# Performance work log

Measured on AMD Instinct MI355X. Metric: run time of the kernel, lower is better.

## Reference

```python
import jax, jax.numpy as jnp
import numpy as np

N, NPG, BS = 32000, 1000, 32
E, H, L, R, K = 512000, 128, 3, 8, 64


def setup_inputs() -> dict:
    key = jax.random.key(0)
    ks = jax.random.split(key, 16)
    sc = 0.05
    x = jax.random.normal(ks[0], (N, H), jnp.float32)
    W_rel = jax.random.normal(ks[1], (L, R, H, H), jnp.float32) * sc
    W_self = jax.random.normal(ks[2], (L, H, H), jnp.float32) * sc
    rel_table = jax.random.normal(ks[3], (R, H), jnp.float32)
    Zn = jax.random.normal(ks[4], (K, H), jnp.float32) * sc
    proj_W = jax.random.normal(ks[5], (L * H, H), jnp.float32) * sc
    proj_b = jnp.zeros((H,), jnp.float32)
    fc_W = jax.random.normal(ks[6], (2 * L * H + 2 * H, 1), jnp.float32) * sc
    fc_b = jnp.zeros((1,), jnp.float32)
    rep_seq = jax.random.normal(ks[7], (BS, H), jnp.float32)
    src = jax.random.randint(ks[8], (E,), 0, N, jnp.int32)
    dst = jax.random.randint(ks[9], (E,), 0, N, jnp.int32)
    etype = jax.random.randint(ks[10], (E,), 0, R, jnp.int32)
    graph_id = (jnp.arange(N, dtype=jnp.int32) // NPG).astype(jnp.int32)
    head_ids = (jnp.arange(BS, dtype=jnp.int32) * NPG)           # node with id==1 per subgraph
    tail_ids = (jnp.arange(BS, dtype=jnp.int32) * NPG + 1)       # node with id==2 per subgraph
    rel_labels = jax.random.randint(ks[11], (BS,), 0, R, jnp.int32)
    return dict(x=x, W_rel=W_rel, W_self=W_self, rel_table=rel_table, Zn=Zn,
                proj_W=proj_W, proj_b=proj_b, fc_W=fc_W, fc_b=fc_b, rep_seq=rep_seq,
                src=src, dst=dst, etype=etype, graph_id=graph_id,
                head_ids=head_ids, tail_ids=tail_ids, rel_labels=rel_labels)


def reference(x, W_rel, W_self, rel_table, Zn, proj_W, proj_b, fc_W, fc_b, rep_seq,
              src, dst, etype, graph_id, head_ids, tail_ids, rel_labels):
    n, h_dim = x.shape
    bs = head_ids.shape[0]
    # RGCN message passing: aggregate src features per (dst, rel), then per-rel linear.
    seg = dst.astype(jnp.int32) * R + etype.astype(jnp.int32)  # [E]
    h = x
    reprs = []
    for l in range(L):
        agg = jax.ops.segment_sum(h[src], seg, num_segments=n * R)  # [N*R, H]
        agg = agg.reshape(n, R, h_dim)
        msg = jnp.einsum('nri,rio->no', agg, W_rel[l])
        h = jax.nn.relu(msg + h @ W_self[l])
        reprs.append(h)
    repr_ = jnp.stack(reprs, axis=1)  # [N, L, H]
    # mean_nodes pooling per subgraph
    counts = jax.ops.segment_sum(jnp.ones((n,), x.dtype), graph_id, num_segments=bs)
    g_mean = jax.ops.segment_sum(repr_, graph_id, num_segments=bs) / counts[:, None, None]
    g_out = jax.nn.leaky_relu(g_mean.reshape(bs, L * h_dim) @ proj_W + proj_b)  # [bs, H]
    # head/tail gathers
    head_flat = repr_[head_ids].reshape(bs, L * h_dim)
    tail_flat = repr_[tail_ids].reshape(bs, L * h_dim)
    rel_embs = rel_table[rel_labels]  # [bs, H]
    h_out = head_flat @ proj_W + proj_b
    t_out = tail_flat @ proj_W + proj_b
    # community view: cluster assignment (softmax) then summary (sigmoid)
    s1 = jax.nn.sigmoid(jax.nn.softmax(h_out @ Zn.T, axis=-1) @ Zn)
    s2 = jax.nn.sigmoid(jax.nn.softmax(t_out @ Zn.T, axis=-1) @ Zn)
    s = s1 * s2
    # view attention aggregation over [subgraph, sequence, community] views
    views = jnp.stack([g_out, rep_seq, s], axis=1)  # [bs, 3, H]
    att = jax.nn.softmax(jnp.sum(rel_embs[:, None, :] * views, axis=-1), axis=-1)  # [bs, 3]
    view_aggr = jnp.sum(att[:, :, None] * views, axis=1)  # [bs, H]
    # positive triplet scoring
    g_rep = jnp.concatenate([head_flat, tail_flat, rel_embs, view_aggr], axis=1)
    out_pos = g_rep @ fc_W + fc_b  # [bs, 1]
    return out_pos
```

## Files before the change

### kernel.cpp

```cpp
#include <hip/hip_runtime.h>

#define N_NODES 32000
#define NPG     1000
#define BSZ     32
#define NEDGE   512000
#define H       128
#define NL      3
#define NR      8
#define NKK     1152
#define NBIN2   262144

typedef __attribute__((ext_vector_type(8))) short short8;
typedef __attribute__((ext_vector_type(4))) float float4v;

__device__ __forceinline__ float bf2f(unsigned short u) {
  union { unsigned int i; float f; } v;
  v.i = ((unsigned int)u) << 16;
  return v.f;
}
__device__ __forceinline__ unsigned short f2bf(float f) {
  union { float f; unsigned int i; } v;
  v.f = f;
  unsigned int x = v.i;
  return (unsigned short)((x + 0x7FFFu + ((x >> 16) & 1u)) >> 16);
}

__device__ __forceinline__ void gl_lds16(const void* g, void* l) {
  __builtin_amdgcn_global_load_lds((__attribute__((address_space(1))) void*)g,
                                   (__attribute__((address_space(3))) void*)l,
                                   16, 0, 0);
}

__global__ __launch_bounds__(256) void k_prep(
    const float* __restrict__ x, const float* __restrict__ W_rel,
    const float* __restrict__ W_self, const int* __restrict__ dst,
    const int* __restrict__ etype, const int* __restrict__ graph_id,
    unsigned short* __restrict__ hb, unsigned short* __restrict__ Bt,
    int* __restrict__ cnt, int* __restrict__ gcount)
{
  const int b = blockIdx.x, t = threadIdx.x;
  if (b < 4000) {
    const size_t i = ((size_t)b * 256 + t) * 4;
    float4 v = *(const float4*)(x + i);
    ushort4 u = { f2bf(v.x), f2bf(v.y), f2bf(v.z), f2bf(v.w) };
    *(ushort4*)(hb + i) = u;
  } else if (b < 5728) {
    const int g = (b - 4000) * 256 + t;
    const int l = g / (H * NKK);
    const int rem = g - l * (H * NKK);
    const int o = rem / NKK;
    const int kk = rem - o * NKK;
    float v = (kk < 1024)
        ? W_rel[(((size_t)l * NR + (kk >> 7)) * H + (kk & 127)) * H + o]
        : W_self[((size_t)l * H + (kk - 1024)) * H + o];
    Bt[g] = f2bf(v);
  } else if (b < 7728) {
    const int e = (b - 5728) * 256 + t;
    atomicAdd(&cnt[dst[e] * 8 + etype[e]], 1);
  } else {
    __shared__ int hist[BSZ];
    if (t < BSZ) hist[t] = 0;
    __syncthreads();
    const int n = (b - 7728) * 256 + t;
    if (n < N_NODES) atomicAdd(&hist[graph_id[n]], 1);
    __syncthreads();
    if (t < BSZ) { int v = hist[t]; if (v) atomicAdd(&gcount[t], v); }
  }
}

__global__ __launch_bounds__(256) void k_scanA(const int* __restrict__ cnt,
                                               int* __restrict__ bsum) {
  __shared__ int red[256];
  const int t = threadIdx.x;
  int4 v = *(const int4*)(cnt + blockIdx.x * 1024 + t * 4);
  red[t] = v.x + v.y + v.z + v.w;
  __syncthreads();
  for (int off = 128; off > 0; off >>= 1) {
    if (t < off) red[t] += red[t + off];
    __syncthreads();
  }
  if (t == 0) bsum[blockIdx.x] = red[0];
}

__global__ __launch_bounds__(256) void k_scanC(const int* __restrict__ cnt,
                                               const int* __restrict__ bsum,
                                               int* __restrict__ row_ptr2,
                                               int* __restrict__ cursor) {
  __shared__ int ts[256], bsx[256];
  const int t = threadIdx.x;
  const int base = blockIdx.x * 1024 + t * 4;
  int4 v = *(const int4*)(cnt + base);
  const int s = v.x + v.y + v.z + v.w;
  ts[t]  = s;
  bsx[t] = bsum[t];
  __syncthreads();
  for (int off = 1; off < 256; off <<= 1) {
    int a = (t >= off) ? ts[t - off]  : 0;
    int c = (t >= off) ? bsx[t - off] : 0;
    __syncthreads();
    ts[t] += a; bsx[t] += c;
    __syncthreads();
  }
  const int boff = (blockIdx.x == 0) ? 0 : bsx[blockIdx.x - 1];
  int ex = ts[t] - s + boff;
  int4 w = { ex, ex + v.x, ex + v.x + v.y, ex + v.x + v.y + v.z };
  *(int4*)(row_ptr2 + base) = w;
  *(int4*)(cursor + base) = w;
}

__global__ void k_fill(const int* __restrict__ src, const int* __restrict__ dst,
                       const int* __restrict__ etype, int* __restrict__ cursor,
                       int* __restrict__ edge_off) {
  int e = blockIdx.x * blockDim.x + threadIdx.x;
  if (e < NEDGE) {
    int p = atomicAdd(&cursor[dst[e] * 8 + etype[e]], 1);
    edge_off[p] = src[e];
  }
}

__global__ __launch_bounds__(256) void k_agg(
    const unsigned short* __restrict__ Hin,
    const int* __restrict__ row_ptr2,
    const int* __restrict__ edge_off,
    unsigned short* __restrict__ A)
{
  const int tid = threadIdx.x;
  const int hw = tid >> 5, li = tid & 31;
  const int nl = hw >> 2, j = hw & 3;
  const int n = blockIdx.x * 2 + nl;
  const unsigned int* Hu = (const unsigned int*)Hin;
  const int rb = n * 8;
  const int b0 = row_ptr2[rb + j],     e0 = row_ptr2[rb + j + 1];
  const int b1 = row_ptr2[rb + j + 4], e1 = row_ptr2[rb + j + 5];
  float a0[4] = {0.f, 0.f, 0.f, 0.f}, a1[4] = {0.f, 0.f, 0.f, 0.f};
  const int steps = max(e0 - b0, e1 - b1);
  for (int it = 0; it < steps; ++it) {
    const int p0 = b0 + it, p1 = b1 + it;
    const bool k0 = p0 < e0, k1 = p1 < e1;
    const int s0 = edge_off[k0 ? p0 : 0];
    const int s1 = edge_off[k1 ? p1 : 0];
    uint2 u0 = *(const uint2*)(Hu + (size_t)s0 * 64 + li * 2);
    uint2 u1 = *(const uint2*)(Hu + (size_t)s1 * 64 + li * 2);
    const unsigned int x0 = k0 ? u0.x : 0u, y0 = k0 ? u0.y : 0u;
    const unsigned int x1 = k1 ? u1.x : 0u, y1 = k1 ? u1.y : 0u;
    a0[0] += bf2f((unsigned short)(x0 & 0xffff));
    a0[1] += bf2f((unsigned short)(x0 >> 16));
    a0[2] += bf2f((unsigned short)(y0 & 0xffff));
    a0[3] += bf2f((unsigned short)(y0 >> 16));
    a1[0] += bf2f((unsigned short)(x1 & 0xffff));
    a1[1] += bf2f((unsigned short)(x1 >> 16));
    a1[2] += bf2f((unsigned short)(y1 & 0xffff));
    a1[3] += bf2f((unsigned short)(y1 >> 16));
  }
  ushort4 w0 = { f2bf(a0[0]), f2bf(a0[1]), f2bf(a0[2]), f2bf(a0[3]) };
  ushort4 w1 = { f2bf(a1[0]), f2bf(a1[1]), f2bf(a1[2]), f2bf(a1[3]) };
  *(ushort4*)(A + (size_t)n * NKK + j * H + li * 4) = w0;
  *(ushort4*)(A + (size_t)n * NKK + (j + 4) * H + li * 4) = w1;
  if (j == 0) {
    uint2 u = *(const uint2*)(Hu + (size_t)n * 64 + li * 2);
    *(uint2*)(A + (size_t)n * NKK + 1024 + li * 4) = u;
  }
}

__global__ __launch_bounds__(512, 2) void k_gemmA(
    const unsigned short* __restrict__ Ag,
    const unsigned short* __restrict__ Bg,
    unsigned short* __restrict__ Hout)
{
  __shared__ __align__(16) unsigned short pool[24576];
  const int tid = threadIdx.x;
  const int w = tid >> 6, lane = tid & 63;
  const int l15 = lane & 15, quad = lane >> 4;
  const int m0 = blockIdx.x * 64;
  const int rbase = (w & 1) * 32;
  const int cbase = (w >> 1) * 32;

  float4v acc[2][2];
  #pragma unroll
  for (int i = 0; i < 2; ++i)
    #pragma unroll
    for (int jj = 0; jj < 2; ++jj) acc[i][jj] = (float4v){0.f, 0.f, 0.f, 0.f};

  {
    int g = tid, row = g >> 3, c = g & 7;
    gl_lds16(Ag + (size_t)(m0 + row) * NKK + ((c ^ (row & 7)) * 8), pool + (size_t)g * 8);
    gl_lds16(Bg + (size_t)row * NKK + ((c ^ (row & 7)) * 8), pool + 4096 + (size_t)g * 8);
    int g2 = tid + 512, row2 = g2 >> 3, c2 = g2 & 7;
    gl_lds16(Bg + (size_t)row2 * NKK + ((c2 ^ (row2 & 7)) * 8), pool + 4096 + (size_t)g2 * 8);
  }
  __syncthreads();

  #pragma unroll 2
  for (int kt = 0; kt < 18; ++kt) {
    const int cur = kt & 1;
    const unsigned short* ac = cur ? pool + 12288 : pool;
    const unsigned short* bc = cur ? pool + 16384 : pool + 4096;
    if (kt < 17) {
      unsigned short* an = cur ? pool : pool + 12288;
      unsigned short* bn = cur ? pool + 4096 : pool + 16384;
      const int kb = (kt + 1) * 64;
      int g = tid, row = g >> 3, c = g & 7;
      gl_lds16(Ag + (size_t)(m0 + row) * NKK + kb + ((c ^ (row & 7)) * 8), an + (size_t)g * 8);
      gl_lds16(Bg + (size_t)row * NKK + kb + ((c ^ (row & 7)) * 8), bn + (size_t)g * 8);
      int g2 = tid + 512, row2 = g2 >> 3, c2 = g2 & 7;
      gl_lds16(Bg + (size_t)row2 * NKK + kb + ((c2 ^ (row2 & 7)) * 8), bn + (size_t)g2 * 8);
    }
    #pragma unroll
    for (int s = 0; s < 2; ++s) {
      short8 af[2], bfv[2];
      #pragma unroll
      for (int rf = 0; rf < 2; ++rf) {
        const int row = rbase + rf * 16 + l15;
        af[rf] = *(const short8*)(ac + row * 64 + (((s * 4 + quad) ^ (row & 7)) * 8));
      }
      #pragma unroll
      for (int cf = 0; cf < 2; ++cf) {
        const int o = cbase + cf * 16 + l15;
        bfv[cf] = *(const short8*)(bc + o * 64 + (((s * 4 + quad) ^ (o & 7)) * 8));
      }
      #pragma unroll
      for (int rf = 0; rf < 2; ++rf)
        #pragma unroll
        for (int cf = 0; cf < 2; ++cf)
          acc[rf][cf] = __builtin_amdgcn_mfma_f32_16x16x32_bf16(af[rf], bfv[cf], acc[rf][cf], 0, 0, 0);
    }
    __syncthreads();
  }

  #pragma unroll
  for (int rf = 0; rf < 2; ++rf)
    #pragma unroll
    for (int cf = 0; cf < 2; ++cf)
      #pragma unroll
      for (int r = 0; r < 4; ++r) {
        const int row = rbase + rf * 16 + quad * 4 + r;
        const int col = cbase + cf * 16 + l15;
        pool[row * 136 + col] = f2bf(fmaxf(acc[rf][cf][r], 0.f));
      }
  __syncthreads();
  #pragma unroll
  for (int rep = 0; rep < 2; ++rep) {
    const int g = rep * 512 + tid;
    const int row = g >> 4, c = g & 15;
    *(uint4*)(Hout + (size_t)(m0 + row) * H + c * 8) = *(const uint4*)(pool + row * 136 + c * 8);
  }
}

__global__ void k_gmean(const unsigned short* __restrict__ hb, float* __restrict__ gmean)
{
  const int g = blockIdx.x, l = blockIdx.y, c = blockIdx.z, t = threadIdx.x;
  const unsigned short* base =
      hb + ((size_t)(l + 1) * N_NODES + (size_t)g * NPG + (size_t)c * (NPG / 8)) * H + t * 2;
  float sx = 0.f, sy = 0.f;
  for (int i = 0; i < 125; ++i) {
    unsigned int u = *(const unsigned int*)(base + (size_t)i * H);
    sx += bf2f((unsigned short)(u & 0xffff));
    sy += bf2f((unsigned short)(u >> 16));
  }
  float* gp = gmean + (size_t)g * (NL * H) + l * H + t * 2;
  atomicAdd(gp, sx);
  atomicAdd(gp + 1, sy);
}

__global__ __launch_bounds__(128) void k_final(
    const unsigned short* __restrict__ hb, const float* __restrict__ gmean,
    const int* __restrict__ gcount,
    const float* __restrict__ rel_tb, const float* __restrict__ Zn,
    const float* __restrict__ projW, const float* __restrict__ projB,
    const float* __restrict__ fcW, const float* __restrict__ fcB,
    const float* __restrict__ repSeq,
    const int* __restrict__ head_ids, const int* __restrict__ tail_ids,
    const int* __restrict__ rel_lab, float* __restrict__ out)
{
  const int b = blockIdx.x;
  const int o = threadIdx.x;
  __shared__ float gm[384], hf[384], tf[384];
  __shared__ float go[128], ho[128], t_o[128], re[128], rs[128], sv[128];
  __shared__ float lg[128], pr[128], red[128], att[3];

  const int hid = head_ids[b], tlid = tail_ids[b], rl = rel_lab[b];
  const float cinv = 1.f / (float)gcount[b];
  #pragma unroll
  for (int l = 0; l < NL; ++l) {
    gm[l * H + o] = gmean[(size_t)b * (NL * H) + l * H + o] * cinv;
    hf[l * H + o] = bf2f(hb[((size_t)(l + 1) * N_NODES + hid) * H + o]);
    tf[l * H + o] = bf2f(hb[((size_t)(l + 1) * N_NODES + tlid) * H + o]);
  }
  re[o] = rel_tb[rl * H + o];
  rs[o] = repSeq[b * H + o];
  __syncthreads();

  float pb = projB[o];
  float sg = pb, sh = pb, st = pb;
  for (int i = 0; i < NL * H; ++i) {
    float wv = projW[i * H + o];
    sg = fmaf(gm[i], wv, sg);
    sh = fmaf(hf[i], wv, sh);
    st = fmaf(tf[i], wv, st);
  }
  go[o] = (sg > 0.f) ? sg : 0.01f * sg;
  ho[o] = sh;
  t_o[o] = st;
  __syncthreads();

  {
    const int k = o & 63;
    const float* v = (o < 64) ? ho : t_o;
    float s = 0.f;
    for (int i = 0; i < H; ++i) s = fmaf(v[i], Zn[k * H + i], s);
    lg[o] = s;
  }
  __syncthreads();
  if (o < 2) {
    float* l0 = &lg[o * 64];
    float* p0 = &pr[o * 64];
    float mx = l0[0];
    for (int k = 1; k < 64; ++k) mx = fmaxf(mx, l0[k]);
    float sum = 0.f;
    for (int k = 0; k < 64; ++k) { float e = __expf(l0[k] - mx); p0[k] = e; sum += e; }
    float inv = 1.f / sum;
    for (int k = 0; k < 64; ++k) p0[k] *= inv;
  }
  __syncthreads();
  {
    float s1 = 0.f, s2 = 0.f;
    for (int k = 0; k < 64; ++k) {
      float z = Zn[k * H + o];
      s1 = fmaf(pr[k], z, s1);
      s2 = fmaf(pr[64 + k], z, s2);
    }
    s1 = 1.f / (1.f + __expf(-s1));
    s2 = 1.f / (1.f + __expf(-s2));
    sv[o] = s1 * s2;
  }
  __syncthreads();
  if (o == 0) {
    float d0 = 0.f, d1 = 0.f, d2 = 0.f;
    for (int i = 0; i < H; ++i) { d0 += re[i] * go[i]; d1 += re[i] * rs[i]; d2 += re[i] * sv[i]; }
    float mx = fmaxf(d0, fmaxf(d1, d2));
    float e0 = __expf(d0 - mx), e1 = __expf(d1 - mx), e2 = __expf(d2 - mx);
    float inv = 1.f / (e0 + e1 + e2);
    att[0] = e0 * inv; att[1] = e1 * inv; att[2] = e2 * inv;
  }
  __syncthreads();
  float va = att[0] * go[o] + att[1] * rs[o] + att[2] * sv[o];

  float p = 0.f;
  p = fmaf(hf[o],       fcW[o],       p);
  p = fmaf(hf[128 + o], fcW[128 + o], p);
  p = fmaf(hf[256 + o], fcW[256 + o], p);
  p = fmaf(tf[o],       fcW[384 + o], p);
  p = fmaf(tf[128 + o], fcW[512 + o], p);
  p = fmaf(tf[256 + o], fcW[640 + o], p);
  p = fmaf(re[o],       fcW[768 + o], p);
  p = fmaf(va,          fcW[896 + o], p);
  red[o] = p;
  __syncthreads();
  if (o == 0) {
    float s = 0.f;
    for (int i = 0; i < 128; ++i) s += red[i];
    out[b] = s + fcB[0];
  }
}

extern "C" void kernel_launch(void* const* d_in, const int* in_sizes, int n_in,
                              void* d_out, int out_size, void* d_ws, size_t ws_size,
                              hipStream_t stream) {
  const float* x        = (const float*)d_in[0];
  const float* W_rel    = (const float*)d_in[1];
  const float* W_self   = (const float*)d_in[2];
  const float* rel_tb   = (const float*)d_in[3];
  const float* Zn       = (const float*)d_in[4];
  const float* proj_W   = (const float*)d_in[5];
  const float* proj_b   = (const float*)d_in[6];
  const float* fc_W     = (const float*)d_in[7];
  const float* fc_b     = (const float*)d_in[8];
  const float* rep_seq  = (const float*)d_in[9];
  const int* src      = (const int*)d_in[10];
  const int* dst      = (const int*)d_in[11];
  const int* etype    = (const int*)d_in[12];
  const int* graph_id = (const int*)d_in[13];
  const int* head_ids = (const int*)d_in[14];
  const int* tail_ids = (const int*)d_in[15];
  const int* rel_lab  = (const int*)d_in[16];
  float* out = (float*)d_out;

  char* w = (char*)d_ws;
  unsigned short* A   = (unsigned short*)w; w += (size_t)N_NODES * NKK * 2;
  unsigned short* hb  = (unsigned short*)w; w += (size_t)(NL + 1) * N_NODES * H * 2;
  unsigned short* Bt2 = (unsigned short*)w; w += (size_t)NL * H * NKK * 2;
  int* row_ptr2 = (int*)w;  w += (size_t)(NBIN2 + 8) * 4;
  int* cursor   = (int*)w;  w += (size_t)NBIN2 * 4;
  int* edge_off = (int*)w;  w += (size_t)NEDGE * 4;
  int* bsum     = (int*)w;  w += (size_t)256 * 4;
  char* z = w;
  int* cnt     = (int*)w;   w += (size_t)NBIN2 * 4;
  int* gcount  = (int*)w;   w += (size_t)32 * 4;
  float* gmean = (float*)w; w += (size_t)BSZ * NL * H * 4;
  size_t zbytes = (size_t)(w - z);

  hipMemsetAsync(z, 0, zbytes, stream);
  k_prep <<<7853, 256, 0, stream>>>(x, W_rel, W_self, dst, etype, graph_id, hb, Bt2, cnt, gcount);
  k_scanA<<<NBIN2 / 1024, 256, 0, stream>>>(cnt, bsum);
  k_scanC<<<NBIN2 / 1024, 256, 0, stream>>>(cnt, bsum, row_ptr2, cursor);
  k_fill <<<NEDGE / 256, 256, 0, stream>>>(src, dst, etype, cursor, edge_off);

  for (int l = 0; l < NL; ++l) {
    const unsigned short* hp = hb + (size_t)l * N_NODES * H;
    unsigned short* hn = hb + (size_t)(l + 1) * N_NODES * H;
    k_agg  <<<N_NODES / 2, 256, 0, stream>>>(hp, row_ptr2, edge_off, A);
    k_gemmA<<<N_NODES / 64, 512, 0, stream>>>(A, Bt2 + (size_t)l * H * NKK, hn);
  }
  k_gmean<<<dim3(BSZ, NL, 8), 64, 0, stream>>>(hb, gmean);
  k_final<<<BSZ, H, 0, stream>>>(hb, gmean, gcount, rel_tb, Zn, proj_W, proj_b, fc_W, fc_b,
                                 rep_seq, head_ids, tail_ids, rel_lab, out);
  (void)in_sizes; (void)n_in; (void)out_size; (void)ws_size;
}
```

Baseline: 356.4 us.

## Unroll gather-aggregation by four per relation and widen GEMM warp tiles

The aggregation kernel now gives each block one node, and each 32-thread group handles one relation. Each group issues four independent edge gathers per iteration instead of interleaving two relations, which raises memory-level parallelism per thread. The GEMM kernel goes from 512 to 256 threads per block, so each wave computes a 32x64 output tile with 8 accumulators. This gives more B-fragment reuse per A load and fewer LDS reads per MFMA, at the cost of more registers per thread. Launch bounds change to allow three blocks per CU.

Result: faster. 343.4 us (-3.6%).

```diff
diff --git a/kernel.cpp b/kernel.cpp
--- a/kernel.cpp
+++ b/kernel.cpp
@@ -125,44 +125,43 @@
     unsigned short* __restrict__ A)
 {
   const int tid = threadIdx.x;
-  const int hw = tid >> 5, li = tid & 31;
-  const int nl = hw >> 2, j = hw & 3;
-  const int n = blockIdx.x * 2 + nl;
+  const int j = tid >> 5;
+  const int li = tid & 31;
+  const int n = blockIdx.x;
   const unsigned int* Hu = (const unsigned int*)Hin;
-  const int rb = n * 8;
-  const int b0 = row_ptr2[rb + j],     e0 = row_ptr2[rb + j + 1];
-  const int b1 = row_ptr2[rb + j + 4], e1 = row_ptr2[rb + j + 5];
-  float a0[4] = {0.f, 0.f, 0.f, 0.f}, a1[4] = {0.f, 0.f, 0.f, 0.f};
-  const int steps = max(e0 - b0, e1 - b1);
-  for (int it = 0; it < steps; ++it) {
-    const int p0 = b0 + it, p1 = b1 + it;
-    const bool k0 = p0 < e0, k1 = p1 < e1;
-    const int s0 = edge_off[k0 ? p0 : 0];
-    const int s1 = edge_off[k1 ? p1 : 0];
-    uint2 u0 = *(const uint2*)(Hu + (size_t)s0 * 64 + li * 2);
-    uint2 u1 = *(const uint2*)(Hu + (size_t)s1 * 64 + li * 2);
-    const unsigned int x0 = k0 ? u0.x : 0u, y0 = k0 ? u0.y : 0u;
-    const unsigned int x1 = k1 ? u1.x : 0u, y1 = k1 ? u1.y : 0u;
-    a0[0] += bf2f((unsigned short)(x0 & 0xffff));
-    a0[1] += bf2f((unsigned short)(x0 >> 16));
-    a0[2] += bf2f((unsigned short)(y0 & 0xffff));
-    a0[3] += bf2f((unsigned short)(y0 >> 16));
-    a1[0] += bf2f((unsigned short)(x1 & 0xffff));
-    a1[1] += bf2f((unsigned short)(x1 >> 16));
-    a1[2] += bf2f((unsigned short)(y1 & 0xffff));
-    a1[3] += bf2f((unsigned short)(y1 >> 16));
-  }
-  ushort4 w0 = { f2bf(a0[0]), f2bf(a0[1]), f2bf(a0[2]), f2bf(a0[3]) };
-  ushort4 w1 = { f2bf(a1[0]), f2bf(a1[1]), f2bf(a1[2]), f2bf(a1[3]) };
-  *(ushort4*)(A + (size_t)n * NKK + j * H + li * 4) = w0;
-  *(ushort4*)(A + (size_t)n * NKK + (j + 4) * H + li * 4) = w1;
+  const int b = row_ptr2[n * 8 + j];
+  const int e = row_ptr2[n * 8 + j + 1];
+  float a0 = 0.f, a1 = 0.f, a2 = 0.f, a3 = 0.f;
+#define ACCW(xx, yy) { \
+    a0 += bf2f((unsigned short)((xx) & 0xffff)); \
+    a1 += bf2f((unsigned short)((xx) >> 16));    \
+    a2 += bf2f((unsigned short)((yy) & 0xffff)); \
+    a3 += bf2f((unsigned short)((yy) >> 16)); }
+  for (int k = b; k < e; k += 4) {
+    const bool v1 = (k + 1) < e, v2 = (k + 2) < e, v3 = (k + 3) < e;
+    const int o0 = edge_off[k];
+    const int o1 = edge_off[v1 ? k + 1 : k];
+    const int o2 = edge_off[v2 ? k + 2 : k];
+    const int o3 = edge_off[v3 ? k + 3 : k];
+    uint2 u0 = *(const uint2*)(Hu + (size_t)o0 * 64 + li * 2);
+    uint2 u1 = *(const uint2*)(Hu + (size_t)o1 * 64 + li * 2);
+    uint2 u2 = *(const uint2*)(Hu + (size_t)o2 * 64 + li * 2);
+    uint2 u3 = *(const uint2*)(Hu + (size_t)o3 * 64 + li * 2);
+    ACCW(u0.x, u0.y)
+    ACCW(v1 ? u1.x : 0u, v1 ? u1.y : 0u)
+    ACCW(v2 ? u2.x : 0u, v2 ? u2.y : 0u)
+    ACCW(v3 ? u3.x : 0u, v3 ? u3.y : 0u)
+  }
+#undef ACCW
+  ushort4 w4 = { f2bf(a0), f2bf(a1), f2bf(a2), f2bf(a3) };
+  *(ushort4*)(A + (size_t)n * NKK + j * H + li * 4) = w4;
   if (j == 0) {
     uint2 u = *(const uint2*)(Hu + (size_t)n * 64 + li * 2);
     *(uint2*)(A + (size_t)n * NKK + 1024 + li * 4) = u;
   }
 }
 
-__global__ __launch_bounds__(512, 2) void k_gemmA(
+__global__ __launch_bounds__(256, 3) void k_gemmA(
     const unsigned short* __restrict__ Ag,
     const unsigned short* __restrict__ Bg,
     unsigned short* __restrict__ Hout)
@@ -173,74 +172,85 @@
   const int l15 = lane & 15, quad = lane >> 4;
   const int m0 = blockIdx.x * 64;
   const int rbase = (w & 1) * 32;
-  const int cbase = (w >> 1) * 32;
-
-  float4v acc[2][2];
+  const int cbase = (w >> 1) * 64;
+
+  float4v acc[2][4];
   #pragma unroll
   for (int i = 0; i < 2; ++i)
     #pragma unroll
-    for (int jj = 0; jj < 2; ++jj) acc[i][jj] = (float4v){0.f, 0.f, 0.f, 0.f};
+    for (int jj = 0; jj < 4; ++jj) acc[i][jj] = (float4v){0.f, 0.f, 0.f, 0.f};
 
   {
-    int g = tid, row = g >> 3, c = g & 7;
-    gl_lds16(Ag + (size_t)(m0 + row) * NKK + ((c ^ (row & 7)) * 8), pool + (size_t)g * 8);
-    gl_lds16(Bg + (size_t)row * NKK + ((c ^ (row & 7)) * 8), pool + 4096 + (size_t)g * 8);
-    int g2 = tid + 512, row2 = g2 >> 3, c2 = g2 & 7;
-    gl_lds16(Bg + (size_t)row2 * NKK + ((c2 ^ (row2 & 7)) * 8), pool + 4096 + (size_t)g2 * 8);
+    #pragma unroll
+    for (int rep = 0; rep < 2; ++rep) {
+      const int g = rep * 256 + tid, row = g >> 3, c = g & 7;
+      gl_lds16(Ag + (size_t)(m0 + row) * NKK + ((c ^ (row & 7)) * 8), pool + (size_t)g * 8);
+    }
+    #pragma unroll
+    for (int rep = 0; rep < 4; ++rep) {
+      const int g = rep * 256 + tid, row = g >> 3, c = g & 7;
+      gl_lds16(Bg + (size_t)row * NKK + ((c ^ (row & 7)) * 8), pool + 4096 + (size_t)g * 8);
+    }
   }
   __syncthreads();
 
   #pragma unroll 2
   for (int kt = 0; kt < 18; ++kt) {
     const int cur = kt & 1;
-    const unsigned short* ac = cur ? pool + 12288 : pool;
-    const unsigned short* bc = cur ? pool + 16384 : pool + 4096;
+    const unsigned short* ac = pool + (cur ? 12288 : 0);
+    const unsigned short* bc = pool + (cur ? 16384 : 4096);
     if (kt < 17) {
-      unsigned short* an = cur ? pool : pool + 12288;
-      unsigned short* bn = cur ? pool + 4096 : pool + 16384;
+      unsigned short* an = pool + (cur ? 0 : 12288);
+      unsigned short* bn = pool + (cur ? 4096 : 16384);
       const int kb = (kt + 1) * 64;
-      int g = tid, row = g >> 3, c = g & 7;
-      gl_lds16(Ag + (size_t)(m0 + row) * NKK + kb + ((c ^ (row & 7)) * 8), an + (size_t)g * 8);
-      gl_lds16(Bg + (size_t)row * NKK + kb + ((c ^ (row & 7)) * 8), bn + (size_t)g * 8);
-      int g2 = tid + 512, row2 = g2 >> 3, c2 = g2 & 7;
-      gl_lds16(Bg + (size_t)row2 * NKK + kb + ((c2 ^ (row2 & 7)) * 8), bn + (size_t)g2 * 8);
+      #pragma unroll
+      for (int rep = 0; rep < 2; ++rep) {
+        const int g = rep * 256 + tid, row = g >> 3, c = g & 7;
+        gl_lds16(Ag + (size_t)(m0 + row) * NKK + kb + ((c ^ (row & 7)) * 8), an + (size_t)g * 8);
+      }
+      #pragma unroll
+      for (int rep = 0; rep < 4; ++rep) {
+        const int g = rep * 256 + tid, row = g >> 3, c = g & 7;
+        gl_lds16(Bg + (size_t)row * NKK + kb + ((c ^ (row & 7)) * 8), bn + (size_t)g * 8);
+      }
     }
     #pragma unroll
     for (int s = 0; s < 2; ++s) {
-      short8 af[2], bfv[2];
-      #pragma unroll
-      for (int rf = 0; rf < 2; ++rf) {
-        const int row = rbase + rf * 16 + l15;
-        af[rf] = *(const short8*)(ac + row * 64 + (((s * 4 + quad) ^ (row & 7)) * 8));
+      const int c = s * 4 + quad;
+      short8 af[2], bfv[4];
+      #pragma unroll
+      for (int i = 0; i < 2; ++i) {
+        const int row = rbase + i * 16 + l15;
+        af[i] = *(const short8*)(ac + row * 64 + ((c ^ (row & 7)) * 8));
       }
       #pragma unroll
-      for (int cf = 0; cf < 2; ++cf) {
-        const int o = cbase + cf * 16 + l15;
-        bfv[cf] = *(const short8*)(bc + o * 64 + (((s * 4 + quad) ^ (o & 7)) * 8));
+      for (int jj = 0; jj < 4; ++jj) {
+        const int orow = cbase + jj * 16 + l15;
+        bfv[jj] = *(const short8*)(bc + orow * 64 + ((c ^ (orow & 7)) * 8));
       }
       #pragma unroll
-      for (int rf = 0; rf < 2; ++rf)
+      for (int i = 0; i < 2; ++i)
         #pragma unroll
-        for (int cf = 0; cf < 2; ++cf)
-          acc[rf][cf] = __builtin_amdgcn_mfma_f32_16x16x32_bf16(af[rf], bfv[cf], acc[rf][cf], 0, 0, 0);
+        for (int jj = 0; jj < 4; ++jj)
+          acc[i][jj] = __builtin_amdgcn_mfma_f32_16x16x32_bf16(af[i], bfv[jj], acc[i][jj], 0, 0, 0);
     }
     __syncthreads();
   }
 
   #pragma unroll
-  for (int rf = 0; rf < 2; ++rf)
+  for (int i = 0; i < 2; ++i)
     #pragma unroll
-    for (int cf = 0; cf < 2; ++cf)
+    for (int jj = 0; jj < 4; ++jj)
       #pragma unroll
       for (int r = 0; r < 4; ++r) {
-        const int row = rbase + rf * 16 + quad * 4 + r;
-        const int col = cbase + cf * 16 + l15;
-        pool[row * 136 + col] = f2bf(fmaxf(acc[rf][cf][r], 0.f));
+        const int row = rbase + i * 16 + quad * 4 + r;
+        const int col = cbase + jj * 16 + l15;
+        pool[row * 136 + col] = f2bf(fmaxf(acc[i][jj][r], 0.f));
       }
   __syncthreads();
   #pragma unroll
-  for (int rep = 0; rep < 2; ++rep) {
-    const int g = rep * 512 + tid;
+  for (int rep = 0; rep < 4; ++rep) {
+    const int g = rep * 256 + tid;
     const int row = g >> 4, c = g & 15;
     *(uint4*)(Hout + (size_t)(m0 + row) * H + c * 8) = *(const uint4*)(pool + row * 136 + c * 8);
   }
@@ -408,8 +418,8 @@
   for (int l = 0; l < NL; ++l) {
     const unsigned short* hp = hb + (size_t)l * N_NODES * H;
     unsigned short* hn = hb + (size_t)(l + 1) * N_NODES * H;
-    k_agg  <<<N_NODES / 2, 256, 0, stream>>>(hp, row_ptr2, edge_off, A);
-    k_gemmA<<<N_NODES / 64, 512, 0, stream>>>(A, Bt2 + (size_t)l * H * NKK, hn);
+    k_agg  <<<N_NODES, 256, 0, stream>>>(hp, row_ptr2, edge_off, A);
+    k_gemmA<<<N_NODES / 64, 256, 0, stream>>>(A, Bt2 + (size_t)l * H * NKK, hn);
   }
   k_gmean<<<dim3(BSZ, NL, 8), 64, 0, stream>>>(hb, gmean);
   k_final<<<BSZ, H, 0, stream>>>(hb, gmean, gcount, rel_tb, Zn, proj_W, proj_b, fc_W, fc_b,
```
